# Kernel optimization log

Measured on AMD Instinct MI355X. Metric: run time of the kernel, lower is better.

The kernel has to match this reference:

```python
import jax, jax.numpy as jnp
import numpy as np

B, N, L = 4, 16, 2048
E = 32768
CH = (64, 128, 128, 128)
EPS = 1e-5


def setup_inputs() -> dict:
    key = jax.random.key(0)
    ks = jax.random.split(key, 6)
    x = jax.random.normal(ks[0], (B, N, CH[0], L), jnp.float32)
    edge_index = jax.random.randint(ks[1], (2, E), 0, L, dtype=jnp.int64)

    def xavier(k, fi, fo):
        std = (2.0 / (fi + fo)) ** 0.5
        return jax.random.normal(k, (fi, fo), jnp.float32) * std

    W1 = xavier(ks[2], CH[0], CH[1])
    W2 = xavier(ks[3], 2 * CH[1], CH[2])
    W3 = xavier(ks[4], 2 * CH[2], CH[3])
    return dict(
        x=x, edge_index=edge_index,
        W1=W1, b1=jnp.zeros((CH[1],), jnp.float32),
        W2=W2, b2=jnp.zeros((CH[2],), jnp.float32),
        W3=W3, b3=jnp.zeros((CH[3],), jnp.float32),
        g1=jnp.ones((2 * CH[1],), jnp.float32), be1=jnp.zeros((2 * CH[1],), jnp.float32),
        g2=jnp.ones((2 * CH[2],), jnp.float32), be2=jnp.zeros((2 * CH[2],), jnp.float32),
        g3=jnp.ones((2 * CH[3],), jnp.float32), be3=jnp.zeros((2 * CH[3],), jnp.float32),
    )


def _gcn_norm(edge_index, l):
    # PyG gcn_norm with improved=True: self loops get weight 2, sym normalization
    src, dst = edge_index[0], edge_index[1]
    loop = jnp.arange(l)
    src_f = jnp.concatenate([src, loop])
    dst_f = jnp.concatenate([dst, loop])
    w = jnp.concatenate([jnp.ones((src.shape[0],), jnp.float32),
                         2.0 * jnp.ones((l,), jnp.float32)])
    deg = jax.ops.segment_sum(w, dst_f, num_segments=l)
    dinv = jnp.where(deg > 0, jax.lax.rsqrt(deg), 0.0)
    return src_f, dst_f, dinv[src_f] * w * dinv[dst_f]


def _gcn(h, W, bias, src, dst, norm):
    # h: [G, l, c_in] -> [G, l, c_out];  out[i] = sum_{j->i} norm_ij * (h_j @ W) + b
    hW = jnp.einsum('glc,cf->glf', h, W)
    msg = hW[:, src, :] * norm[None, :, None]
    out = jnp.zeros_like(hW).at[:, dst, :].add(msg)
    return out + bias


def _block(h, W, bias, g, beta, src, dst, norm, b, n, l):
    # h: [b, n, l, c_in]
    a = _gcn(h.reshape(b * n, l, h.shape[-1]), W, bias, src, dst, norm)
    a = a.reshape(b, n, l, -1)
    amax = a.max(axis=1, keepdims=True)
    a = jnp.concatenate([a, jnp.broadcast_to(amax, a.shape)], axis=-1)  # [b,n,l,2c]
    # BatchNorm1d training stats over (b, n, l) per channel (biased var)
    mean = a.mean(axis=(0, 1, 2))
    var = a.var(axis=(0, 1, 2))
    return jax.nn.relu((a - mean) * jax.lax.rsqrt(var + EPS) * g + beta)


def reference(x, edge_index, W1, b1, W2, b2, W3, b3, g1, be1, g2, be2, g3, be3):
    b, n, c, l = x.shape
    h = jnp.transpose(x, (0, 1, 3, 2))  # [b, n, l, c] node-major
    src, dst, norm = _gcn_norm(edge_index, l)
    h = _block(h, W1, b1, g1, be1, src, dst, norm, b, n, l)
    h = _block(h, W2, b2, g2, be2, src, dst, norm, b, n, l)
    h = _block(h, W3, b3, g3, be3, src, dst, norm, b, n, l)
    # match torch output layout [b*n, 2*channels[3], l]
    return jnp.transpose(h.reshape(b * n, l, -1), (0, 2, 1))
```

## Files before the change

kernel.cpp:

```cpp
#include <hip/hip_runtime.h>
#include <hip/hip_bf16.h>
#include <cstddef>
#include <cstdint>

#define BB 4
#define NN 16
#define GG 64
#define LL 2048
#define EE 32768
#define EF (EE + LL)
#define C0 64
#define CC 256
#define EPS 1e-5f

typedef __bf16 bf16x8 __attribute__((ext_vector_type(8)));
typedef __bf16 bf16x4 __attribute__((ext_vector_type(4)));
typedef __bf16 bf16x2 __attribute__((ext_vector_type(2)));
typedef float f32x4 __attribute__((ext_vector_type(4)));

struct __align__(8) Edge { int col; float val; };


__global__ void detect_kernel(const int* __restrict__ ei, int* __restrict__ flag) {
    int t = threadIdx.x;
    int bad = 0;
    for (int i = t; i < 256; i += 64) bad |= (ei[2 * i + 1] != 0) ? 1 : 0;
    int any = __any(bad);
    if (t == 0) *flag = any ? 0 : 1;
}

__global__ void prep_init_kernel(const void* __restrict__ ei, const int* __restrict__ flag,
                                 int* __restrict__ e32, float* __restrict__ deg,
                                 int* __restrict__ cnt, float* __restrict__ sums) {
    int i = blockIdx.x * 256 + threadIdx.x;
    if (i < 2 * EE) {
        int v;
        if (*flag)
            v = (int)((const long long*)ei)[i];
        else
            v = ((const int*)ei)[i];
        e32[i] = v;
    }
    if (i < LL) { deg[i] = 2.0f; cnt[i] = 1; }
    if (i < 512) sums[i] = 0.0f;
}

__global__ void deg_kernel(const int* __restrict__ e32, float* __restrict__ deg,
                           int* __restrict__ cnt) {
    int e = blockIdx.x * 256 + threadIdx.x;
    if (e >= EE) return;
    int d = e32[EE + e];
    atomicAdd(&deg[d], 1.0f);
    atomicAdd(&cnt[d], 1);
}

__global__ void scan_dinv_kernel(const int* __restrict__ cnt, const float* __restrict__ deg,
                                 int* __restrict__ rowptr, int* __restrict__ cursor,
                                 float* __restrict__ dinv) {
    __shared__ int part[256];
    int t = threadIdx.x;
    int base = t * 8;
    int loc[8];
    int s = 0;
#pragma unroll
    for (int j = 0; j < 8; ++j) {
        loc[j] = s; s += cnt[base + j];
        dinv[base + j] = rsqrtf(deg[base + j]);
    }
    part[t] = s;
    __syncthreads();
    if (t == 0) {
        int run = 0;
        for (int i = 0; i < 256; ++i) { int v = part[i]; part[i] = run; run += v; }
    }
    __syncthreads();
    int off = part[t];
#pragma unroll
    for (int j = 0; j < 8; ++j) {
        int rp = off + loc[j];
        rowptr[base + j] = rp;
        cursor[base + j] = rp;
    }
    if (t == 255) rowptr[LL] = off + s;
}

__global__ void fill_kernel(const int* __restrict__ e32, const float* __restrict__ dinv,
                            int* __restrict__ cursor, Edge* __restrict__ edges) {
    int idx = blockIdx.x * 256 + threadIdx.x;
    if (idx >= EF) return;
    int s, d; float w;
    if (idx < EE) {
        s = e32[idx]; d = e32[EE + idx];
        w = dinv[s] * dinv[d];
    } else {
        int i = idx - EE;
        s = i; d = i;
        w = 2.0f * dinv[i] * dinv[i];
    }
    int pos = atomicAdd(&cursor[d], 1);
    edges[pos].col = s;
    edges[pos].val = w;
}


__global__ void prep_w_all(const float* __restrict__ W0, const float* __restrict__ W1,
                           const float* __restrict__ W2, __bf16* __restrict__ Wf0,
                           __bf16* __restrict__ Wf1, __bf16* __restrict__ Wf2) {
    int t = blockIdx.x * 256 + threadIdx.x;
    const float* W; __bf16* Wf;
    if (t < 1024)      { W = W0; Wf = Wf0; }
    else if (t < 5120) { W = W1; Wf = Wf1; t -= 1024; }
    else if (t < 9216) { W = W2; Wf = Wf2; t -= 5120; }
    else return;
    int lane = t & 63;
    int rest = t >> 6;
    int n16 = rest & 7;
    int ks = rest >> 3;
    int col = n16 * 16 + (lane & 15);
    int k0 = ks * 32 + (lane >> 4) * 8;
    bf16x8 v;
#pragma unroll
    for (int j = 0; j < 8; ++j) v[j] = (__bf16)W[(size_t)(k0 + j) * 128 + col];
    *(bf16x8*)(Wf + (size_t)t * 8) = v;
}


__global__ void transpose_x(const float* __restrict__ x, float* __restrict__ h) {
    __shared__ float t[32][33];
    int g = blockIdx.z, c0 = blockIdx.y * 32, l0 = blockIdx.x * 32;
    int tx = threadIdx.x, ty = threadIdx.y;
    const float* xp = x + ((size_t)g * C0 + c0) * LL + l0;
#pragma unroll
    for (int i = ty; i < 32; i += 8) t[i][tx] = xp[(size_t)i * LL + tx];
    __syncthreads();
    float* hp = h + ((size_t)g * LL + l0) * C0 + c0;
#pragma unroll
    for (int i = ty; i < 32; i += 8) hp[(size_t)i * C0 + tx] = t[tx][i];
}


template <int K, bool BN>
__global__ __launch_bounds__(256) void gemm_mfma(const float* __restrict__ A0,
                                                 const float* __restrict__ amax,
                                                 const float* __restrict__ scb,
                                                 const __bf16* __restrict__ Wf,
                                                 __bf16* __restrict__ hw) {
    const int g = blockIdx.y;
    const int l0 = blockIdx.x * 64;
    const int tid = threadIdx.x;
    const int wid = tid >> 6;
    const int lane = tid & 63;
    __shared__ __align__(16) __bf16 As[64 * 64];

    f32x4 acc[8];
#pragma unroll
    for (int nf = 0; nf < 8; ++nf) acc[nf] = (f32x4){0.f, 0.f, 0.f, 0.f};

    for (int kt = 0; kt < K / 64; ++kt) {
#pragma unroll
        for (int it = 0; it < 4; ++it) {
            int f4 = tid + it * 256;
            int row = f4 >> 4;
            int kq = (f4 & 15) * 4;
            int gk = kt * 64 + kq;
            float4 v;
            if constexpr (BN) {
                if (gk < 128)
                    v = *(const float4*)(A0 + ((size_t)g * LL + l0 + row) * 128 + gk);
                else
                    v = *(const float4*)(amax + ((size_t)(g >> 4) * LL + l0 + row) * 128 + (gk - 128));
                float4 s = *(const float4*)(scb + gk);
                float4 b = *(const float4*)(scb + 256 + gk);
                v.x = fmaxf(fmaf(v.x, s.x, b.x), 0.f);
                v.y = fmaxf(fmaf(v.y, s.y, b.y), 0.f);
                v.z = fmaxf(fmaf(v.z, s.z, b.z), 0.f);
                v.w = fmaxf(fmaf(v.w, s.w, b.w), 0.f);
            } else {
                v = *(const float4*)(A0 + ((size_t)g * LL + l0 + row) * 64 + gk);
            }
            int sidx = row * 64 + (kq ^ ((row & 7) << 3));
            bf16x4 pv = {(__bf16)v.x, (__bf16)v.y, (__bf16)v.z, (__bf16)v.w};
            *(bf16x4*)(&As[sidx]) = pv;
        }
        __syncthreads();
#pragma unroll
        for (int ks2 = 0; ks2 < 2; ++ks2) {
            const int row = wid * 16 + (lane & 15);
            const int kk = ks2 * 32 + (lane >> 4) * 8;
            bf16x8 af = *(const bf16x8*)(&As[row * 64 + (kk ^ ((row & 7) << 3))]);
            const int ksg = kt * 2 + ks2;
            const __bf16* wp = Wf + (size_t)ksg * 8 * 512 + lane * 8;
#pragma unroll
            for (int nf = 0; nf < 8; ++nf) {
                bf16x8 bfr = *(const bf16x8*)(wp + nf * 512);
                acc[nf] = __builtin_amdgcn_mfma_f32_16x16x32_bf16(af, bfr, acc[nf], 0, 0, 0);
            }
        }
        __syncthreads();
    }
    __bf16* op = hw + ((size_t)g * LL + l0) * 128;
#pragma unroll
    for (int nf = 0; nf < 8; ++nf) {
        int col = nf * 16 + (lane & 15);
#pragma unroll
        for (int j = 0; j < 4; ++j) {
            int row = wid * 16 + (lane >> 4) * 4 + j;
            op[(size_t)row * 128 + col] = (__bf16)acc[nf][j];
        }
    }
}


__global__ __launch_bounds__(256) void agg_kernel(const __bf16* __restrict__ hw,
                                                  const float* __restrict__ bias,
                                                  const int* __restrict__ rowptr,
                                                  const Edge* __restrict__ edges,
                                                  float* __restrict__ aout) {
    const int lane = threadIdx.x & 63;
    const int grp = lane >> 4;
    const int ch16 = lane & 15;
    const int bid = blockIdx.x;
    const int xcd = bid & 7;
    const int slot = bid >> 3;
    const int gswz = ((slot >> 9) << 3) + xcd;
    const int within = slot & 511;
    int node = (gswz << 11) + within * 4 + (threadIdx.x >> 6);
    node = __builtin_amdgcn_readfirstlane(node);
    const int g = node >> 11, l = node & (LL - 1);
    const __bf16* __restrict__ base = hw + (size_t)g * LL * 128 + ch16 * 8;
    const int j0 = rowptr[l];
    const int deg = rowptr[l + 1] - j0;

    float acc[8];
#pragma unroll
    for (int j = 0; j < 8; ++j) acc[j] = 0.0f;

    for (int d0 = 0; d0 < deg; d0 += 64) {
        const int cnt = min(64, deg - d0);
        Edge e;
        e.col = 0; e.val = 0.0f;
        if (lane < cnt) e = edges[j0 + d0 + lane];
        int d = 0;
        for (; d + 8 <= cnt; d += 8) {
            int i1 = d + grp, i2 = d + 4 + grp;
            int c1 = __shfl(e.col, i1); float w1 = __shfl(e.val, i1);
            int c2 = __shfl(e.col, i2); float w2 = __shfl(e.val, i2);
            bf16x8 v1 = *(const bf16x8*)(base + (size_t)c1 * 128);
            bf16x8 v2 = *(const bf16x8*)(base + (size_t)c2 * 128);
#pragma unroll
            for (int j = 0; j < 8; ++j) acc[j] = fmaf(w1, (float)v1[j], acc[j]);
#pragma unroll
            for (int j = 0; j < 8; ++j) acc[j] = fmaf(w2, (float)v2[j], acc[j]);
        }
        for (; d < cnt; d += 4) {
            int i1 = d + grp;
            int c1 = __shfl(e.col, i1); float w1 = __shfl(e.val, i1);
            bf16x8 v1 = *(const bf16x8*)(base + (size_t)c1 * 128);
#pragma unroll
            for (int j = 0; j < 8; ++j) acc[j] = fmaf(w1, (float)v1[j], acc[j]);
        }
    }
#pragma unroll
    for (int j = 0; j < 8; ++j) {
        acc[j] += __shfl_xor(acc[j], 16);
        acc[j] += __shfl_xor(acc[j], 32);
    }
    if (grp == 0) {
        float4 b0 = *(const float4*)(bias + ch16 * 8);
        float4 b1 = *(const float4*)(bias + ch16 * 8 + 4);
        float4 s0 = make_float4(acc[0] + b0.x, acc[1] + b0.y, acc[2] + b0.z, acc[3] + b0.w);
        float4 s1 = make_float4(acc[4] + b1.x, acc[5] + b1.y, acc[6] + b1.z, acc[7] + b1.w);
        float* op = aout + (size_t)node * 128 + ch16 * 8;
        *(float4*)op = s0;
        *(float4*)(op + 4) = s1;
    }
}


__global__ void maxstats_kernel(const float* __restrict__ a, float* __restrict__ amax,
                                float* __restrict__ sums, float* __restrict__ sumsq) {
    int bb = blockIdx.x >> 7;
    int lt = blockIdx.x & 127;
    int l0 = lt * 16;
    int f = threadIdx.x;
    float s = 0.f, ss = 0.f, sa = 0.f, ssa = 0.f;
    for (int li = 0; li < 16; ++li) {
        int l = l0 + li;
        float m = -3.402823466e38f;
#pragma unroll
        for (int n = 0; n < NN; ++n) {
            float v = a[(((size_t)(bb * NN + n) * LL + l) * 128) + f];
            m = fmaxf(m, v);
            s += v;
            ss = fmaf(v, v, ss);
        }
        amax[((size_t)bb * LL + l) * 128 + f] = m;
        sa += m;
        ssa = fmaf(m, m, ssa);
    }
    atomicAdd(&sums[f], s);
    atomicAdd(&sumsq[f], ss);
    atomicAdd(&sums[128 + f], sa);
    atomicAdd(&sumsq[128 + f], ssa);
}

__global__ void bnfinal_kernel(float* __restrict__ sums, float* __restrict__ sumsq,
                               const float* __restrict__ gamma, const float* __restrict__ beta,
                               float* __restrict__ scb) {
    int f = threadIdx.x;
    float cntv = (f < 128) ? (float)(BB * NN * LL) : (float)(BB * LL);
    float mean = sums[f] / cntv;
    float var = sumsq[f] / cntv - mean * mean;
    float s = gamma[f] * rsqrtf(var + EPS);
    scb[f] = s;
    scb[256 + f] = beta[f] - mean * s;
    sums[f] = 0.0f;
    sumsq[f] = 0.0f;
}


__global__ void transpose_norm_out(const float* __restrict__ a, const float* __restrict__ amax,
                                   const float* __restrict__ scb, float* __restrict__ out) {
    __shared__ float t[64][65];
    int g = blockIdx.z, f0 = blockIdx.y * 64, l0 = blockIdx.x * 64;
    int tx = threadIdx.x, ty = threadIdx.y;
    int f = f0 + tx;
    float s = scb[f], b = scb[256 + f];
#pragma unroll
    for (int i = ty; i < 64; i += 8) {
        int l = l0 + i;
        float v;
        if (f0 < 128)
            v = a[((size_t)g * LL + l) * 128 + f];
        else
            v = amax[((size_t)(g >> 4) * LL + l) * 128 + (f - 128)];
        t[i][tx] = fmaxf(fmaf(v, s, b), 0.f);
    }
    __syncthreads();
    float* op = out + ((size_t)g * CC + f0) * LL + l0;
#pragma unroll
    for (int i = ty; i < 64; i += 8) op[(size_t)i * LL + tx] = t[tx][i];
}


extern "C" void kernel_launch(void* const* d_in, const int* in_sizes, int n_in,
                              void* d_out, int out_size, void* d_ws, size_t ws_size,
                              hipStream_t stream) {
    const float* x = (const float*)d_in[0];
    const void* ei = d_in[1];
    const float* W[3] = {(const float*)d_in[2], (const float*)d_in[4], (const float*)d_in[6]};
    const float* bia[3] = {(const float*)d_in[3], (const float*)d_in[5], (const float*)d_in[7]};
    const float* gam[3] = {(const float*)d_in[8], (const float*)d_in[10], (const float*)d_in[12]};
    const float* bet[3] = {(const float*)d_in[9], (const float*)d_in[11], (const float*)d_in[13]};
    float* out = (float*)d_out;

    char* w = (char*)d_ws;
    float* h0   = (float*)w;  w += (size_t)GG * LL * C0 * 4;
    float* a    = (float*)w;  w += (size_t)GG * LL * 128 * 4;
    __bf16* hw  = (__bf16*)w; w += (size_t)GG * LL * 128 * 2;
    float* amax = (float*)w;  w += (size_t)BB * LL * 128 * 4;
    __bf16* Wf[3];
    Wf[0] = (__bf16*)w; w += 65536 * 2;
    Wf[1] = (__bf16*)w; w += 65536 * 2;
    Wf[2] = (__bf16*)w; w += 65536 * 2;
    int*   e32   = (int*)w;    w += (size_t)2 * EE * 4;
    float* deg   = (float*)w;  w += LL * 4;
    int*   cnt   = (int*)w;    w += LL * 4;
    int*   rowptr= (int*)w;    w += (LL + 4) * 4;
    int*   cursor= (int*)w;    w += LL * 4;
    Edge*  edges = (Edge*)w;   w += (size_t)EF * 8;
    float* dinv  = (float*)w;  w += LL * 4;
    float* sums  = (float*)w;  w += 256 * 4;
    float* sumsq = (float*)w;  w += 256 * 4;
    float* scb   = (float*)w;  w += 512 * 4;
    int*   flag  = (int*)w;    w += 256;

    detect_kernel<<<1, 64, 0, stream>>>((const int*)ei, flag);
    prep_init_kernel<<<(2 * EE + 255) / 256, 256, 0, stream>>>(ei, flag, e32, deg, cnt, sums);
    deg_kernel<<<(EE + 255) / 256, 256, 0, stream>>>(e32, deg, cnt);
    scan_dinv_kernel<<<1, 256, 0, stream>>>(cnt, deg, rowptr, cursor, dinv);
    fill_kernel<<<(EF + 255) / 256, 256, 0, stream>>>(e32, dinv, cursor, edges);

    prep_w_all<<<36, 256, 0, stream>>>(W[0], W[1], W[2], Wf[0], Wf[1], Wf[2]);

    transpose_x<<<dim3(LL / 32, C0 / 32, GG), dim3(32, 8), 0, stream>>>(x, h0);

    gemm_mfma<64, false><<<dim3(LL / 64, GG), 256, 0, stream>>>(h0, amax, scb, Wf[0], hw);
    agg_kernel<<<GG * LL / 4, 256, 0, stream>>>(hw, bia[0], rowptr, edges, a);
    maxstats_kernel<<<BB * (LL / 16), 128, 0, stream>>>(a, amax, sums, sumsq);
    bnfinal_kernel<<<1, 256, 0, stream>>>(sums, sumsq, gam[0], bet[0], scb);

    gemm_mfma<256, true><<<dim3(LL / 64, GG), 256, 0, stream>>>(a, amax, scb, Wf[1], hw);
    agg_kernel<<<GG * LL / 4, 256, 0, stream>>>(hw, bia[1], rowptr, edges, a);
    maxstats_kernel<<<BB * (LL / 16), 128, 0, stream>>>(a, amax, sums, sumsq);
    bnfinal_kernel<<<1, 256, 0, stream>>>(sums, sumsq, gam[1], bet[1], scb);

    gemm_mfma<256, true><<<dim3(LL / 64, GG), 256, 0, stream>>>(a, amax, scb, Wf[2], hw);
    agg_kernel<<<GG * LL / 4, 256, 0, stream>>>(hw, bia[2], rowptr, edges, a);
    maxstats_kernel<<<BB * (LL / 16), 128, 0, stream>>>(a, amax, sums, sumsq);
    bnfinal_kernel<<<1, 256, 0, stream>>>(sums, sumsq, gam[2], bet[2], scb);

    transpose_norm_out<<<dim3(LL / 64, CC / 64, GG), dim3(64, 8), 0, stream>>>(a, amax, scb, out);
}
```

Before: 531.6 us.

## Fuse max/BN stats into aggregation with node-interleaved hw layout

New measurement: 596.4 us. 1.12x slower.

```diff
diff --git a/kernel.cpp b/kernel.cpp
--- a/kernel.cpp
+++ b/kernel.cpp
@@ -15,41 +15,42 @@
 
 typedef __bf16 bf16x8 __attribute__((ext_vector_type(8)));
 typedef __bf16 bf16x4 __attribute__((ext_vector_type(4)));
-typedef __bf16 bf16x2 __attribute__((ext_vector_type(2)));
 typedef float f32x4 __attribute__((ext_vector_type(4)));
 
 struct __align__(8) Edge { int col; float val; };
 
 
-__global__ void detect_kernel(const int* __restrict__ ei, int* __restrict__ flag) {
-    int t = threadIdx.x;
-    int bad = 0;
-    for (int i = t; i < 256; i += 64) bad |= (ei[2 * i + 1] != 0) ? 1 : 0;
-    int any = __any(bad);
-    if (t == 0) *flag = any ? 0 : 1;
-}
-
-__global__ void prep_init_kernel(const void* __restrict__ ei, const int* __restrict__ flag,
-                                 int* __restrict__ e32, float* __restrict__ deg,
-                                 int* __restrict__ cnt, float* __restrict__ sums) {
+__global__ void detect_init_kernel(const int* __restrict__ ei, int* __restrict__ flag,
+                                   float* __restrict__ deg, int* __restrict__ cnt,
+                                   float* __restrict__ gstats) {
     int i = blockIdx.x * 256 + threadIdx.x;
-    if (i < 2 * EE) {
-        int v;
-        if (*flag)
-            v = (int)((const long long*)ei)[i];
-        else
-            v = ((const int*)ei)[i];
-        e32[i] = v;
-    }
     if (i < LL) { deg[i] = 2.0f; cnt[i] = 1; }
-    if (i < 512) sums[i] = 0.0f;
-}
-
-__global__ void deg_kernel(const int* __restrict__ e32, float* __restrict__ deg,
-                           int* __restrict__ cnt) {
+    gstats[i * 2] = 0.0f;
+    gstats[i * 2 + 1] = 0.0f;
+    if (blockIdx.x == 0 && threadIdx.x < 64) {
+        int t = threadIdx.x;
+        int bad = 0;
+        for (int k = t; k < 256; k += 64) bad |= (ei[2 * k + 1] != 0) ? 1 : 0;
+        int any = __any(bad);
+        if (t == 0) *flag = any ? 0 : 1;
+    }
+}
+
+__global__ void conv_deg_kernel(const void* __restrict__ ei, const int* __restrict__ flag,
+                                int* __restrict__ e32, float* __restrict__ deg,
+                                int* __restrict__ cnt) {
     int e = blockIdx.x * 256 + threadIdx.x;
     if (e >= EE) return;
-    int d = e32[EE + e];
+    int s, d;
+    if (*flag) {
+        s = (int)((const long long*)ei)[e];
+        d = (int)((const long long*)ei)[EE + e];
+    } else {
+        s = ((const int*)ei)[e];
+        d = ((const int*)ei)[EE + e];
+    }
+    e32[e] = s;
+    e32[EE + e] = d;
     atomicAdd(&deg[d], 1.0f);
     atomicAdd(&cnt[d], 1);
 }
@@ -150,7 +151,8 @@
     const int tid = threadIdx.x;
     const int wid = tid >> 6;
     const int lane = tid & 63;
-    __shared__ __align__(16) __bf16 As[64 * 64];
+    __shared__ __align__(16) float smem[64 * 132];
+    __bf16* As = (__bf16*)smem;
 
     f32x4 acc[8];
 #pragma unroll
@@ -198,124 +200,198 @@
         }
         __syncthreads();
     }
-    __bf16* op = hw + ((size_t)g * LL + l0) * 128;
 #pragma unroll
     for (int nf = 0; nf < 8; ++nf) {
         int col = nf * 16 + (lane & 15);
 #pragma unroll
         for (int j = 0; j < 4; ++j) {
             int row = wid * 16 + (lane >> 4) * 4 + j;
-            op[(size_t)row * 128 + col] = (__bf16)acc[nf][j];
-        }
-    }
-}
-
-
-__global__ __launch_bounds__(256) void agg_kernel(const __bf16* __restrict__ hw,
-                                                  const float* __restrict__ bias,
-                                                  const int* __restrict__ rowptr,
-                                                  const Edge* __restrict__ edges,
-                                                  float* __restrict__ aout) {
-    const int lane = threadIdx.x & 63;
-    const int grp = lane >> 4;
-    const int ch16 = lane & 15;
+            smem[row * 132 + col] = acc[nf][j];
+        }
+    }
+    __syncthreads();
+    const int b_ = g >> 4, n_ = g & 15;
+    const int half_ = n_ >> 3, n8_ = n_ & 7;
+    const int row = tid >> 2, seg = tid & 3;
+    __bf16* dst = hw + ((size_t)((b_ * LL + l0 + row) * 2 + half_) * 8 + n8_) * 128 + seg * 32;
+    const float* src = smem + row * 132 + seg * 32;
+#pragma unroll
+    for (int q = 0; q < 4; ++q) {
+        bf16x8 o;
+#pragma unroll
+        for (int i = 0; i < 8; ++i) o[i] = (__bf16)src[q * 8 + i];
+        *(bf16x8*)(dst + q * 8) = o;
+    }
+}
+
+
+__global__ __launch_bounds__(256) void agg_half(const __bf16* __restrict__ hw,
+                                                const float* __restrict__ bias,
+                                                const int* __restrict__ rowptr,
+                                                const Edge* __restrict__ edges,
+                                                float* __restrict__ a,
+                                                float* __restrict__ halfmax,
+                                                float* __restrict__ gstats) {
+    __shared__ float bl_sum[128], bl_ssq[128];
+    const int tid = threadIdx.x;
+    if (tid < 128) { bl_sum[tid] = 0.f; bl_ssq[tid] = 0.f; }
+    __syncthreads();
+
     const int bid = blockIdx.x;
     const int xcd = bid & 7;
-    const int slot = bid >> 3;
-    const int gswz = ((slot >> 9) << 3) + xcd;
-    const int within = slot & 511;
-    int node = (gswz << 11) + within * 4 + (threadIdx.x >> 6);
-    node = __builtin_amdgcn_readfirstlane(node);
-    const int g = node >> 11, l = node & (LL - 1);
-    const __bf16* __restrict__ base = hw + (size_t)g * LL * 128 + ch16 * 8;
+    const int b = xcd >> 1, half = xcd & 1;
+    const int lgrp = bid >> 3;
+    const int l = lgrp * 4 + (tid >> 6);
+    const int lane = tid & 63;
+    const int n8 = lane >> 3;
+    const int chs = lane & 7;
+
+    const __bf16* __restrict__ base =
+        hw + (size_t)b * LL * 2048 + (size_t)(half * 8 + n8) * 128 + chs * 16;
     const int j0 = rowptr[l];
     const int deg = rowptr[l + 1] - j0;
 
-    float acc[8];
-#pragma unroll
-    for (int j = 0; j < 8; ++j) acc[j] = 0.0f;
+    float acc[16];
+#pragma unroll
+    for (int i = 0; i < 16; ++i) acc[i] = 0.0f;
 
     for (int d0 = 0; d0 < deg; d0 += 64) {
-        const int cnt = min(64, deg - d0);
+        const int cntE = min(64, deg - d0);
         Edge e;
         e.col = 0; e.val = 0.0f;
-        if (lane < cnt) e = edges[j0 + d0 + lane];
+        if (lane < cntE) e = edges[j0 + d0 + lane];
         int d = 0;
-        for (; d + 8 <= cnt; d += 8) {
-            int i1 = d + grp, i2 = d + 4 + grp;
-            int c1 = __shfl(e.col, i1); float w1 = __shfl(e.val, i1);
-            int c2 = __shfl(e.col, i2); float w2 = __shfl(e.val, i2);
-            bf16x8 v1 = *(const bf16x8*)(base + (size_t)c1 * 128);
-            bf16x8 v2 = *(const bf16x8*)(base + (size_t)c2 * 128);
-#pragma unroll
-            for (int j = 0; j < 8; ++j) acc[j] = fmaf(w1, (float)v1[j], acc[j]);
-#pragma unroll
-            for (int j = 0; j < 8; ++j) acc[j] = fmaf(w2, (float)v2[j], acc[j]);
-        }
-        for (; d < cnt; d += 4) {
-            int i1 = d + grp;
-            int c1 = __shfl(e.col, i1); float w1 = __shfl(e.val, i1);
-            bf16x8 v1 = *(const bf16x8*)(base + (size_t)c1 * 128);
-#pragma unroll
-            for (int j = 0; j < 8; ++j) acc[j] = fmaf(w1, (float)v1[j], acc[j]);
-        }
-    }
-#pragma unroll
-    for (int j = 0; j < 8; ++j) {
-        acc[j] += __shfl_xor(acc[j], 16);
-        acc[j] += __shfl_xor(acc[j], 32);
-    }
-    if (grp == 0) {
-        float4 b0 = *(const float4*)(bias + ch16 * 8);
-        float4 b1 = *(const float4*)(bias + ch16 * 8 + 4);
-        float4 s0 = make_float4(acc[0] + b0.x, acc[1] + b0.y, acc[2] + b0.z, acc[3] + b0.w);
-        float4 s1 = make_float4(acc[4] + b1.x, acc[5] + b1.y, acc[6] + b1.z, acc[7] + b1.w);
-        float* op = aout + (size_t)node * 128 + ch16 * 8;
-        *(float4*)op = s0;
-        *(float4*)(op + 4) = s1;
-    }
-}
-
-
-__global__ void maxstats_kernel(const float* __restrict__ a, float* __restrict__ amax,
-                                float* __restrict__ sums, float* __restrict__ sumsq) {
-    int bb = blockIdx.x >> 7;
-    int lt = blockIdx.x & 127;
-    int l0 = lt * 16;
-    int f = threadIdx.x;
-    float s = 0.f, ss = 0.f, sa = 0.f, ssa = 0.f;
-    for (int li = 0; li < 16; ++li) {
-        int l = l0 + li;
-        float m = -3.402823466e38f;
-#pragma unroll
-        for (int n = 0; n < NN; ++n) {
-            float v = a[(((size_t)(bb * NN + n) * LL + l) * 128) + f];
-            m = fmaxf(m, v);
-            s += v;
-            ss = fmaf(v, v, ss);
-        }
-        amax[((size_t)bb * LL + l) * 128 + f] = m;
-        sa += m;
-        ssa = fmaf(m, m, ssa);
-    }
-    atomicAdd(&sums[f], s);
-    atomicAdd(&sumsq[f], ss);
-    atomicAdd(&sums[128 + f], sa);
-    atomicAdd(&sumsq[128 + f], ssa);
-}
-
-__global__ void bnfinal_kernel(float* __restrict__ sums, float* __restrict__ sumsq,
+        for (; d + 2 <= cntE; d += 2) {
+            int c1 = __shfl(e.col, d);     float w1 = __shfl(e.val, d);
+            int c2 = __shfl(e.col, d + 1); float w2 = __shfl(e.val, d + 1);
+            const __bf16* p1 = base + (size_t)c1 * 2048;
+            const __bf16* p2 = base + (size_t)c2 * 2048;
+            bf16x8 va = *(const bf16x8*)p1;
+            bf16x8 vb = *(const bf16x8*)(p1 + 8);
+            bf16x8 vc = *(const bf16x8*)p2;
+            bf16x8 vd = *(const bf16x8*)(p2 + 8);
+#pragma unroll
+            for (int i = 0; i < 8; ++i) {
+                acc[i]     = fmaf(w1, (float)va[i], acc[i]);
+                acc[8 + i] = fmaf(w1, (float)vb[i], acc[8 + i]);
+            }
+#pragma unroll
+            for (int i = 0; i < 8; ++i) {
+                acc[i]     = fmaf(w2, (float)vc[i], acc[i]);
+                acc[8 + i] = fmaf(w2, (float)vd[i], acc[8 + i]);
+            }
+        }
+        if (d < cntE) {
+            int c1 = __shfl(e.col, d); float w1 = __shfl(e.val, d);
+            const __bf16* p1 = base + (size_t)c1 * 2048;
+            bf16x8 va = *(const bf16x8*)p1;
+            bf16x8 vb = *(const bf16x8*)(p1 + 8);
+#pragma unroll
+            for (int i = 0; i < 8; ++i) {
+                acc[i]     = fmaf(w1, (float)va[i], acc[i]);
+                acc[8 + i] = fmaf(w1, (float)vb[i], acc[8 + i]);
+            }
+        }
+    }
+
+#pragma unroll
+    for (int q = 0; q < 4; ++q) {
+        float4 bv = *(const float4*)(bias + chs * 16 + q * 4);
+        acc[q * 4 + 0] += bv.x; acc[q * 4 + 1] += bv.y;
+        acc[q * 4 + 2] += bv.z; acc[q * 4 + 3] += bv.w;
+    }
+
+    {
+        float* ap = a + ((size_t)(b * 16 + half * 8 + n8) * LL + l) * 128 + chs * 16;
+#pragma unroll
+        for (int q = 0; q < 4; ++q)
+            *(float4*)(ap + q * 4) = make_float4(acc[q * 4], acc[q * 4 + 1],
+                                                 acc[q * 4 + 2], acc[q * 4 + 3]);
+    }
+
+    float mx[16], sm[16], sq[16];
+#pragma unroll
+    for (int i = 0; i < 16; ++i) { mx[i] = acc[i]; sm[i] = acc[i]; sq[i] = acc[i] * acc[i]; }
+#pragma unroll
+    for (int st = 8; st <= 32; st <<= 1) {
+#pragma unroll
+        for (int i = 0; i < 16; ++i) {
+            mx[i] = fmaxf(mx[i], __shfl_xor(mx[i], st));
+            sm[i] += __shfl_xor(sm[i], st);
+            sq[i] += __shfl_xor(sq[i], st);
+        }
+    }
+
+    if (n8 == 0) {
+        float* hp = halfmax + ((size_t)(b * 2 + half) * LL + l) * 128 + chs * 16;
+#pragma unroll
+        for (int q = 0; q < 4; ++q)
+            *(float4*)(hp + q * 4) = make_float4(mx[q * 4], mx[q * 4 + 1],
+                                                 mx[q * 4 + 2], mx[q * 4 + 3]);
+#pragma unroll
+        for (int i = 0; i < 16; ++i) {
+            atomicAdd(&bl_sum[chs * 16 + i], sm[i]);
+            atomicAdd(&bl_ssq[chs * 16 + i], sq[i]);
+        }
+    }
+    __syncthreads();
+    const int slot = lgrp & 7;
+    if (tid < 128)
+        atomicAdd(&gstats[slot * 512 + tid], bl_sum[tid]);
+    else if (tid < 256)
+        atomicAdd(&gstats[slot * 512 + 256 + (tid - 128)], bl_ssq[tid - 128]);
+}
+
+
+__global__ void combine_kernel(const float* __restrict__ halfmax, float* __restrict__ amax,
+                               float* __restrict__ gstats) {
+    __shared__ float ls[256], lq[256];
+    const int tid = threadIdx.x;
+    const int idx = blockIdx.x * 256 + tid;
+    const int ch = idx & 127;
+    const int rest = idx >> 7;
+    const int b = rest >> 9, lgrp = rest & 511;
+    float s = 0.f, q = 0.f;
+#pragma unroll
+    for (int i = 0; i < 4; ++i) {
+        int l = lgrp * 4 + i;
+        float m0 = halfmax[((size_t)(b * 2 + 0) * LL + l) * 128 + ch];
+        float m1 = halfmax[((size_t)(b * 2 + 1) * LL + l) * 128 + ch];
+        float m = fmaxf(m0, m1);
+        amax[((size_t)b * LL + l) * 128 + ch] = m;
+        s += m;
+        q = fmaf(m, m, q);
+    }
+    ls[tid] = s; lq[tid] = q;
+    __syncthreads();
+    if (tid < 128) {
+        s = ls[tid] + ls[tid + 128];
+        q = lq[tid] + lq[tid + 128];
+        int slot = blockIdx.x & 7;
+        atomicAdd(&gstats[slot * 512 + 128 + tid], s);
+        atomicAdd(&gstats[slot * 512 + 256 + 128 + tid], q);
+    }
+}
+
+
+__global__ void bnfinal_kernel(float* __restrict__ gstats,
                                const float* __restrict__ gamma, const float* __restrict__ beta,
                                float* __restrict__ scb) {
     int f = threadIdx.x;
+    float sm = 0.f, sq = 0.f;
+#pragma unroll
+    for (int s = 0; s < 8; ++s) {
+        sm += gstats[s * 512 + f];
+        sq += gstats[s * 512 + 256 + f];
+        gstats[s * 512 + f] = 0.f;
+        gstats[s * 512 + 256 + f] = 0.f;
+    }
     float cntv = (f < 128) ? (float)(BB * NN * LL) : (float)(BB * LL);
-    float mean = sums[f] / cntv;
-    float var = sumsq[f] / cntv - mean * mean;
+    float mean = sm / cntv;
+    float var = sq / cntv - mean * mean;
     float s = gamma[f] * rsqrtf(var + EPS);
     scb[f] = s;
     scb[256 + f] = beta[f] - mean * s;
-    sums[f] = 0.0f;
-    sumsq[f] = 0.0f;
 }
 
 
@@ -355,50 +431,48 @@
     float* out = (float*)d_out;
 
     char* w = (char*)d_ws;
-    float* h0   = (float*)w;  w += (size_t)GG * LL * C0 * 4;
-    float* a    = (float*)w;  w += (size_t)GG * LL * 128 * 4;
-    __bf16* hw  = (__bf16*)w; w += (size_t)GG * LL * 128 * 2;
-    float* amax = (float*)w;  w += (size_t)BB * LL * 128 * 4;
+    float* h0     = (float*)w;  w += (size_t)GG * LL * C0 * 4;
+    float* a      = (float*)w;  w += (size_t)GG * LL * 128 * 4;
+    __bf16* hw    = (__bf16*)w; w += (size_t)GG * LL * 128 * 2;
+    float* amax   = (float*)w;  w += (size_t)BB * LL * 128 * 4;
+    float* halfmax= (float*)w;  w += (size_t)BB * 2 * LL * 128 * 4;
     __bf16* Wf[3];
     Wf[0] = (__bf16*)w; w += 65536 * 2;
     Wf[1] = (__bf16*)w; w += 65536 * 2;
     Wf[2] = (__bf16*)w; w += 65536 * 2;
-    int*   e32   = (int*)w;    w += (size_t)2 * EE * 4;
-    float* deg   = (float*)w;  w += LL * 4;
-    int*   cnt   = (int*)w;    w += LL * 4;
-    int*   rowptr= (int*)w;    w += (LL + 4) * 4;
-    int*   cursor= (int*)w;    w += LL * 4;
-    Edge*  edges = (Edge*)w;   w += (size_t)EF * 8;
-    float* dinv  = (float*)w;  w += LL * 4;
-    float* sums  = (float*)w;  w += 256 * 4;
-    float* sumsq = (float*)w;  w += 256 * 4;
-    float* scb   = (float*)w;  w += 512 * 4;
-    int*   flag  = (int*)w;    w += 256;
-
-    detect_kernel<<<1, 64, 0, stream>>>((const int*)ei, flag);
-    prep_init_kernel<<<(2 * EE + 255) / 256, 256, 0, stream>>>(ei, flag, e32, deg, cnt, sums);
-    deg_kernel<<<(EE + 255) / 256, 256, 0, stream>>>(e32, deg, cnt);
+    int*   e32    = (int*)w;    w += (size_t)2 * EE * 4;
+    float* deg    = (float*)w;  w += LL * 4;
+    int*   cnt    = (int*)w;    w += LL * 4;
+    int*   rowptr = (int*)w;    w += (LL + 4) * 4;
+    int*   cursor = (int*)w;    w += LL * 4;
+    Edge*  edges  = (Edge*)w;   w += (size_t)EF * 8;
+    float* dinv   = (float*)w;  w += LL * 4;
+    float* gstats = (float*)w;  w += 8 * 512 * 4;
+    float* scb    = (float*)w;  w += 512 * 4;
+    int*   flag   = (int*)w;    w += 256;
+
+    detect_init_kernel<<<8, 256, 0, stream>>>((const int*)ei, flag, deg, cnt, gstats);
+    conv_deg_kernel<<<(EE + 255) / 256, 256, 0, stream>>>(ei, flag, e32, deg, cnt);
     scan_dinv_kernel<<<1, 256, 0, stream>>>(cnt, deg, rowptr, cursor, dinv);
     fill_kernel<<<(EF + 255) / 256, 256, 0, stream>>>(e32, dinv, cursor, edges);
 
     prep_w_all<<<36, 256, 0, stream>>>(W[0], W[1], W[2], Wf[0], Wf[1], Wf[2]);
-
     transpose_x<<<dim3(LL / 32, C0 / 32, GG), dim3(32, 8), 0, stream>>>(x, h0);
 
     gemm_mfma<64, false><<<dim3(LL / 64, GG), 256, 0, stream>>>(h0, amax, scb, Wf[0], hw);
-    agg_kernel<<<GG * LL / 4, 256, 0, stream>>>(hw, bia[0], rowptr, edges, a);
-    maxstats_kernel<<<BB * (LL / 16), 128, 0, stream>>>(a, amax, sums, sumsq);
-    bnfinal_kernel<<<1, 256, 0, stream>>>(sums, sumsq, gam[0], bet[0], scb);
+    agg_half<<<4096, 256, 0, stream>>>(hw, bia[0], rowptr, edges, a, halfmax, gstats);
+    combine_kernel<<<1024, 256, 0, stream>>>(halfmax, amax, gstats);
+    bnfinal_kernel<<<1, 256, 0, stream>>>(gstats, gam[0], bet[0], scb);
 
     gemm_mfma<256, true><<<dim3(LL / 64, GG), 256, 0, stream>>>(a, amax, scb, Wf[1], hw);
-    agg_kernel<<<GG * LL / 4, 256, 0, stream>>>(hw, bia[1], rowptr, edges, a);
-    maxstats_kernel<<<BB * (LL / 16), 128, 0, stream>>>(a, amax, sums, sumsq);
-    bnfinal_kernel<<<1, 256, 0, stream>>>(sums, sumsq, gam[1], bet[1], scb);
+    agg_half<<<4096, 256, 0, stream>>>(hw, bia[1], rowptr, edges, a, halfmax, gstats);
+    combine_kernel<<<1024, 256, 0, stream>>>(halfmax, amax, gstats);
+    bnfinal_kernel<<<1, 256, 0, stream>>>(gstats, gam[1], bet[1], scb);
 
     gemm_mfma<256, true><<<dim3(LL / 64, GG), 256, 0, stream>>>(a, amax, scb, Wf[2], hw);
-    agg_kernel<<<GG * LL / 4, 256, 0, stream>>>(hw, bia[2], rowptr, edges, a);
-    maxstats_kernel<<<BB * (LL / 16), 128, 0, stream>>>(a, amax, sums, sumsq);
-    bnfinal_kernel<<<1, 256, 0, stream>>>(sums, sumsq, gam[2], bet[2], scb);
+    agg_half<<<4096, 256, 0, stream>>>(hw, bia[2], rowptr, edges, a, halfmax, gstats);
+    combine_kernel<<<1024, 256, 0, stream>>>(halfmax, amax, gstats);
+    bnfinal_kernel<<<1, 256, 0, stream>>>(gstats, gam[2], bet[2], scb);
 
     transpose_norm_out<<<dim3(LL / 64, CC / 64, GG), dim3(64, 8), 0, stream>>>(a, amax, scb, out);
 }
```
